# Optimization experiments

Hardware: AMD Instinct MI355X
Metric: run time of the kernel (lower is better)

The kernel has to match this reference:

```python
import jax, jax.numpy as jnp
import numpy as np

KNN_K = 3
EPS = 1e-8


def _make_poses(key, batch):
    """Random valid SE(3) matrices [B,4,4] (rotation via QR, small translation)."""
    k1, k2 = jax.random.split(key)
    A = jax.random.normal(k1, (batch, 3, 3), dtype=jnp.float32)
    Q, _ = jnp.linalg.qr(A)
    det = jnp.linalg.det(Q)[:, None, None]
    Q = Q * jnp.where(det < 0, -1.0, 1.0)  # ensure proper rotation
    t = jax.random.normal(k2, (batch, 3), dtype=jnp.float32) * 0.5
    pose = jnp.tile(jnp.eye(4, dtype=jnp.float32), (batch, 1, 1))
    pose = pose.at[:, :3, :3].set(Q)
    pose = pose.at[:, :3, 3].set(t)
    return pose


def setup_inputs() -> dict:
    key = jax.random.key(0)
    kq, kr, kf, kp0, kp1 = jax.random.split(key, 5)
    B, N, M = 2, 8192, 8192
    pc0 = jax.random.normal(kq, (B, N, 3), dtype=jnp.float32) * 20.0
    pc1 = jax.random.normal(kr, (B, M, 3), dtype=jnp.float32) * 20.0
    flow1 = jax.random.normal(kf, (B, M, 3), dtype=jnp.float32)
    pose0 = _make_poses(kp0, B)
    pose1 = _make_poses(kp1, B)
    return {"pc0": pc0, "pc1": pc1, "flow1": flow1, "pose0": pose0, "pose1": pose1}


def reference(pc0, pc1, flow1, pose0, pose1):
    # cal_pose0to1: transform from pc0 ego frame into pc1 ego frame
    pose_0to1 = jnp.linalg.inv(pose1) @ pose0            # [B,4,4]
    R = pose_0to1[:, :3, :3]                             # [B,3,3]
    t = pose_0to1[:, :3, 3]                              # [B,3]
    # pc0_in_pc1 = pc0 @ R^T + t
    pc0_t = jnp.einsum("bij,bnj->bni", R, pc0) + t[:, None, :]  # [B,N,3]
    pose_flow = pc0_t - pc0                              # ego-motion displacement

    # pairwise squared distances (cdist^2) via GEMM form: [B,N,M]
    q2 = jnp.sum(pc0_t * pc0_t, axis=-1)                 # [B,N]
    r2 = jnp.sum(pc1 * pc1, axis=-1)                     # [B,M]
    cross = jnp.einsum("bnd,bmd->bnm", pc0_t, pc1)
    d2 = q2[:, :, None] + r2[:, None, :] - 2.0 * cross

    # KNN: k smallest distances
    neg_d2, idx = jax.lax.top_k(-d2, KNN_K)              # [B,N,k]
    d = jnp.sqrt(jnp.maximum(-neg_d2, 0.0))

    # inverse-distance weights over the k neighbors
    w = 1.0 / (d + EPS)
    w = w / jnp.sum(w, axis=-1, keepdims=True)           # [B,N,k]

    # gather neighbor flows: flow1 [B,M,3] -> [B,N,k,3]
    gathered = jnp.take_along_axis(flow1[:, None, :, :], idx[..., None], axis=2)
    flow_interp = jnp.sum(w[..., None] * gathered, axis=2)  # [B,N,3]
    return flow_interp, pose_flow
```

## Files before the change

### kernel.cpp

```cpp
#include <hip/hip_runtime.h>
#include <math.h>
#include <float.h>
#include <limits.h>

#define CS   128
#define CT   16
#define TILE_PTS (CT * CS)
#define CSP  129
#define QB1  64
#define QT   16
#define MARGIN 0.05f
typedef unsigned long long ull;
#define KMAX 0xFFFFFFFFFFFFFFFFull

__device__ __forceinline__ unsigned int ford(float f) {
    unsigned int b = __float_as_uint(f);
    return b ^ (((unsigned int)((int)b >> 31)) | 0x80000000u);
}
__device__ __forceinline__ float funord(unsigned int u) {
    unsigned int m = ((u >> 31) - 1u) | 0x80000000u;
    return __uint_as_float(u ^ m);
}

__device__ __forceinline__ ull umin64(ull a, ull b) { return a < b ? a : b; }
__device__ __forceinline__ ull umax64(ull a, ull b) { return a > b ? a : b; }

__device__ __forceinline__ void ins3k(ull k, ull& k0, ull& k1, ull& k2) {
    ull n2 = umax64(k1, umin64(k2, k));
    ull n1 = umax64(k0, umin64(k1, k));
    k0 = umin64(k0, k);
    k1 = n1;
    k2 = n2;
}

__device__ __forceinline__ void sins(float d, float& a0, float& a1, float& a2)
{
    float n1 = __builtin_amdgcn_fmed3f(a0, a1, d);
    float n2 = __builtin_amdgcn_fmed3f(a1, a2, d);
    a0 = fminf(a0, d);
    a1 = n1;
    a2 = n2;
}

__device__ __forceinline__ void pose_rel(const float* __restrict__ P0,
                                         const float* __restrict__ P1,
                                         float R[3][3], float tv[3])
{
    float dt0 = P0[3]  - P1[3];
    float dt1 = P0[7]  - P1[7];
    float dt2 = P0[11] - P1[11];
    #pragma unroll
    for (int i = 0; i < 3; ++i) {
        float a0 = P1[i], a1 = P1[4 + i], a2 = P1[8 + i];
        #pragma unroll
        for (int j = 0; j < 3; ++j)
            R[i][j] = fmaf(a2, P0[8 + j], fmaf(a1, P0[4 + j], a0 * P0[j]));
        tv[i] = fmaf(a2, dt2, fmaf(a1, dt1, a0 * dt0));
    }
}

__launch_bounds__(256, 4)
__global__ void knn_phaseA(const float* __restrict__ pc0,
                           const float* __restrict__ pc1,
                           const float* __restrict__ pose0,
                           const float* __restrict__ pose1,
                           float* __restrict__ cmin,
                           int B, int N, int M, int cstride)
{
    __shared__ float4 tile[CT * CSP];
    __shared__ float4 qd[QB1];

    const int tid = threadIdx.x;
    const int b   = blockIdx.z;
    const int ctb = blockIdx.y;
    const int qb  = blockIdx.x * QB1;
    const int pbase = ctb * TILE_PTS;

    if (tid < QB1) {
        float R[3][3], tv[3];
        pose_rel(pose0 + b * 16, pose1 + b * 16, R, tv);
        int qg0 = qb + tid;
        int qg  = (qg0 < N) ? qg0 : (N - 1);
        const float px = pc0[(size_t)(b * N + qg) * 3 + 0];
        const float py = pc0[(size_t)(b * N + qg) * 3 + 1];
        const float pz = pc0[(size_t)(b * N + qg) * 3 + 2];
        float qx = fmaf(R[0][2], pz, fmaf(R[0][1], py, R[0][0] * px)) + tv[0];
        float qy = fmaf(R[1][2], pz, fmaf(R[1][1], py, R[1][0] * px)) + tv[1];
        float qz = fmaf(R[2][2], pz, fmaf(R[2][1], py, R[2][0] * px)) + tv[2];
        qd[tid] = make_float4(qx, qy, qz,
                              (qx * qx + qy * qy) + qz * qz);
    }

    #pragma unroll
    for (int k = 0; k < TILE_PTS / (256 * 4); ++k) {
        const int pl = (tid + k * 256) * 4;
        const int p  = pbase + pl;
        float4* dst = &tile[(pl >> 7) * CSP + (pl & (CS - 1))];
        if (p + 3 < M) {
            const float4* pf = (const float4*)(pc1 + (size_t)(b * M + p) * 3);
            float4 A = pf[0], Bv = pf[1], C = pf[2];
            dst[0] = make_float4(-2.f * A.x, -2.f * A.y, -2.f * A.z,
                                 (A.x * A.x + A.y * A.y) + A.z * A.z);
            dst[1] = make_float4(-2.f * A.w, -2.f * Bv.x, -2.f * Bv.y,
                                 (A.w * A.w + Bv.x * Bv.x) + Bv.y * Bv.y);
            dst[2] = make_float4(-2.f * Bv.z, -2.f * Bv.w, -2.f * C.x,
                                 (Bv.z * Bv.z + Bv.w * Bv.w) + C.x * C.x);
            dst[3] = make_float4(-2.f * C.y, -2.f * C.z, -2.f * C.w,
                                 (C.y * C.y + C.z * C.z) + C.w * C.w);
        } else {
            #pragma unroll
            for (int u = 0; u < 4; ++u) {
                int pp = p + u;
                float4 v;
                if (pp < M) {
                    const float* s = pc1 + (size_t)(b * M + pp) * 3;
                    float x = s[0], y = s[1], z = s[2];
                    v = make_float4(-2.f * x, -2.f * y, -2.f * z,
                                    (x * x + y * y) + z * z);
                } else {
                    v = make_float4(0.f, 0.f, 0.f, FLT_MAX);
                }
                dst[u] = v;
            }
        }
    }
    __syncthreads();

    const int w    = tid >> 6;
    const int lane = tid & 63;
    const int cl   = lane & 15;
    const int part = lane >> 4;

    float4 qv[QT];
    #pragma unroll
    for (int t = 0; t < QT; ++t) qv[t] = qd[w * QT + t];

    float mm[QT];
    #pragma unroll
    for (int t = 0; t < QT; ++t) mm[t] = FLT_MAX;

    const float4* tp = &tile[cl * CSP + part * 32];
    #pragma unroll 4
    for (int i = 0; i < 32; ++i) {
        const float4 v = tp[i];
        #pragma unroll
        for (int t = 0; t < QT; ++t)
            mm[t] = fminf(mm[t],
                fmaf(qv[t].x, v.x, fmaf(qv[t].y, v.y, fmaf(qv[t].z, v.z, v.w))));
    }

    #pragma unroll
    for (int msk = 16; msk <= 32; msk <<= 1) {
        #pragma unroll
        for (int t = 0; t < QT; ++t)
            mm[t] = fminf(mm[t], __shfl_xor(mm[t], msk));
    }

    if (part == 0) {
        const int cg = ctb * CT + cl;
        #pragma unroll
        for (int t = 0; t < QT; ++t) {
            int qg0 = qb + w * QT + t;
            int qg  = (qg0 < N) ? qg0 : (N - 1);
            cmin[((size_t)b * N + qg) * cstride + cg] = mm[t];
        }
    }
}

__launch_bounds__(256, 8)
__global__ void knn_select(const float* __restrict__ pc0,
                           const float* __restrict__ pc1,
                           const float* __restrict__ flow1,
                           const float* __restrict__ pose0,
                           const float* __restrict__ pose1,
                           const float* __restrict__ cmin,
                           float* __restrict__ out,
                           int B, int N, int M, int cstride)
{
    const int tid  = threadIdx.x;
    const int w    = tid >> 6;
    const int lane = tid & 63;
    const int g    = lane >> 4;
    const int l    = lane & 15;
    const int b    = blockIdx.y;
    const int q0   = blockIdx.x * 16 + w * 4 + g;
    const bool qvalid = (q0 < N);
    const int q    = qvalid ? q0 : (N - 1);

    const int ncc = cstride;
    const size_t row = (size_t)(b * N + q) * cstride;
    float c0, c1, c2, c3;
    if (l * 4 + 3 < ncc) {
        float4 cv = *(const float4*)&cmin[row + l * 4];
        c0 = cv.x; c1 = cv.y; c2 = cv.z; c3 = cv.w;
    } else {
        c0 = (l * 4 + 0 < ncc) ? cmin[row + l * 4 + 0] : FLT_MAX;
        c1 = (l * 4 + 1 < ncc) ? cmin[row + l * 4 + 1] : FLT_MAX;
        c2 = (l * 4 + 2 < ncc) ? cmin[row + l * 4 + 2] : FLT_MAX;
        c3 = (l * 4 + 3 < ncc) ? cmin[row + l * 4 + 3] : FLT_MAX;
    }

    float R[3][3], tv[3];
    pose_rel(pose0 + b * 16, pose1 + b * 16, R, tv);
    const float px = pc0[(size_t)(b * N + q) * 3 + 0];
    const float py = pc0[(size_t)(b * N + q) * 3 + 1];
    const float pz = pc0[(size_t)(b * N + q) * 3 + 2];
    const float qx = fmaf(R[0][2], pz, fmaf(R[0][1], py, R[0][0] * px)) + tv[0];
    const float qy = fmaf(R[1][2], pz, fmaf(R[1][1], py, R[1][0] * px)) + tv[1];
    const float qz = fmaf(R[2][2], pz, fmaf(R[2][1], py, R[2][0] * px)) + tv[2];
    const float q2 = (qx * qx + qy * qy) + qz * qz;

    float a0 = FLT_MAX, a1 = FLT_MAX, a2 = FLT_MAX;
    sins(c0, a0, a1, a2);
    sins(c1, a0, a1, a2);
    sins(c2, a0, a1, a2);
    sins(c3, a0, a1, a2);
    #pragma unroll
    for (int msk = 1; msk <= 8; msk <<= 1) {
        float o0 = __shfl_xor(a0, msk);
        float o1 = __shfl_xor(a1, msk);
        float o2 = __shfl_xor(a2, msk);
        sins(o0, a0, a1, a2);
        sins(o1, a0, a1, a2);
        sins(o2, a0, a1, a2);
    }
    const float thr = a2 + MARGIN;

    ull mask = ((ull)(c0 <= thr) << (4 * l + 0))
             | ((ull)(c1 <= thr) << (4 * l + 1))
             | ((ull)(c2 <= thr) << (4 * l + 2))
             | ((ull)(c3 <= thr) << (4 * l + 3));
    #pragma unroll
    for (int msk = 1; msk <= 8; msk <<= 1)
        mask |= __shfl_xor(mask, msk);

    ull kA0 = KMAX, kA1 = KMAX, kA2 = KMAX;
    ull kB0 = KMAX, kB1 = KMAX, kB2 = KMAX;
    while (mask) {
        const int ck = (int)__builtin_ctzll(mask);
        mask &= mask - 1;
        #pragma unroll
        for (int r = 0; r < CS / 16; ++r) {
            const int m = ck * CS + r * 16 + l;
            if (m < M) {
                const float* pp = pc1 + (size_t)(b * M + m) * 3;
                float x = pp[0], y = pp[1], z = pp[2];
                float r2 = (x * x + y * y) + z * z;
                float cr = fmaf(qz, z, fmaf(qy, y, qx * x));
                float dd = fmaf(-2.0f, cr, q2 + r2);
                ull kk = ((ull)ford(dd) << 32) | (unsigned int)m;
                if (r & 1) ins3k(kk, kB0, kB1, kB2);
                else       ins3k(kk, kA0, kA1, kA2);
            }
        }
    }
    ins3k(kB0, kA0, kA1, kA2);
    ins3k(kB1, kA0, kA1, kA2);
    ins3k(kB2, kA0, kA1, kA2);

    #pragma unroll
    for (int msk = 1; msk <= 8; msk <<= 1) {
        ull o0 = __shfl_xor(kA0, msk);
        ull o1 = __shfl_xor(kA1, msk);
        ull o2 = __shfl_xor(kA2, msk);
        ins3k(o0, kA0, kA1, kA2);
        ins3k(o1, kA0, kA1, kA2);
        ins3k(o2, kA0, kA1, kA2);
    }

    if (l == 0 && qvalid) {
        size_t pf = (size_t)B * N * 3 + (size_t)(b * N + q) * 3;
        out[pf + 0] = qx - px;
        out[pf + 1] = qy - py;
        out[pf + 2] = qz - pz;

        float D0 = funord((unsigned int)(kA0 >> 32));
        float D1 = funord((unsigned int)(kA1 >> 32));
        float D2 = funord((unsigned int)(kA2 >> 32));
        int   i0 = (int)(unsigned int)kA0;
        int   i1 = (int)(unsigned int)kA1;
        int   i2 = (int)(unsigned int)kA2;

        float dd0 = sqrtf(fmaxf(D0, 0.f));
        float dd1 = sqrtf(fmaxf(D1, 0.f));
        float dd2 = sqrtf(fmaxf(D2, 0.f));
        float w0 = 1.0f / (dd0 + 1e-8f);
        float w1 = 1.0f / (dd1 + 1e-8f);
        float w2 = 1.0f / (dd2 + 1e-8f);
        float wsum = (w0 + w1) + w2;
        w0 /= wsum; w1 /= wsum; w2 /= wsum;

        const float* f0 = flow1 + (size_t)(b * M + i0) * 3;
        const float* f1 = flow1 + (size_t)(b * M + i1) * 3;
        const float* f2 = flow1 + (size_t)(b * M + i2) * 3;

        const size_t ob = (size_t)(b * N + q) * 3;
        #pragma unroll
        for (int c = 0; c < 3; ++c) {
            float p0 = w0 * f0[c];
            float p1 = w1 * f1[c];
            float p2 = w2 * f2[c];
            out[ob + c] = (p0 + p1) + p2;
        }
    }
}

extern "C" void kernel_launch(void* const* d_in, const int* in_sizes, int n_in,
                              void* d_out, int out_size, void* d_ws, size_t ws_size,
                              hipStream_t stream) {
    const float* pc0   = (const float*)d_in[0];
    const float* pc1   = (const float*)d_in[1];
    const float* flow1 = (const float*)d_in[2];
    const float* pose0 = (const float*)d_in[3];
    const float* pose1 = (const float*)d_in[4];
    float* out = (float*)d_out;

    const int B = in_sizes[3] / 16;
    const int N = in_sizes[0] / (3 * B);
    const int M = in_sizes[1] / (3 * B);

    const int nct     = (M + TILE_PTS - 1) / TILE_PTS;
    const int cstride = nct * CT;

    float* cmin = (float*)d_ws;

    dim3 g1((N + QB1 - 1) / QB1, nct, B);
    knn_phaseA<<<g1, dim3(256), 0, stream>>>(pc0, pc1, pose0, pose1,
                                             cmin, B, N, M, cstride);

    dim3 g2((N + 15) / 16, B);
    knn_select<<<g2, dim3(256), 0, stream>>>(pc0, pc1, flow1, pose0, pose1,
                                             cmin, out, B, N, M, cstride);
}
```

Measured before the change: 34.07 us.

## Refine KNN pruning to 32-point sub-chunks with precomputed float4 point tile

Phase A now writes a per-query minimum for each 32-point sub-chunk instead of each 128-point chunk, and the first query block also stores the transformed pc1 points (-2x, -2y, -2z, r2) into a float4 workspace. The select kernel builds a small per-query list of candidate sub-chunks in shared memory with atomics and scans only those, reading the precomputed float4 points. If the list overflows it falls back to scanning every point. The aim is fewer candidate distance evaluations and cheaper loads in the select pass. In exchange, phase A writes four times as many minima and skips its shuffle reduction, and the select pass adds atomics and a brute-force fallback path.

```diff
diff --git a/kernel.cpp b/kernel.cpp
--- a/kernel.cpp
+++ b/kernel.cpp
@@ -4,11 +4,13 @@
 #include <limits.h>
 
 #define CS   128
+#define SUBS 32
 #define CT   16
 #define TILE_PTS (CT * CS)
 #define CSP  129
 #define QB1  64
 #define QT   16
+#define LCAP 12
 #define MARGIN 0.05f
 typedef unsigned long long ull;
 #define KMAX 0xFFFFFFFFFFFFFFFFull
@@ -64,8 +66,9 @@
                            const float* __restrict__ pc1,
                            const float* __restrict__ pose0,
                            const float* __restrict__ pose1,
-                           float* __restrict__ cmin,
-                           int B, int N, int M, int cstride)
+                           float* __restrict__ submin,
+                           float4* __restrict__ ptile,
+                           int B, int N, int M, int nsub)
 {
     __shared__ float4 tile[CT * CSP];
     __shared__ float4 qd[QB1];
@@ -91,36 +94,49 @@
                               (qx * qx + qy * qy) + qz * qz);
     }
 
+    const bool wr = (blockIdx.x == 0);
     #pragma unroll
     for (int k = 0; k < TILE_PTS / (256 * 4); ++k) {
         const int pl = (tid + k * 256) * 4;
         const int p  = pbase + pl;
         float4* dst = &tile[(pl >> 7) * CSP + (pl & (CS - 1))];
+        float4 w0, w1, w2, w3;
         if (p + 3 < M) {
             const float4* pf = (const float4*)(pc1 + (size_t)(b * M + p) * 3);
             float4 A = pf[0], Bv = pf[1], C = pf[2];
-            dst[0] = make_float4(-2.f * A.x, -2.f * A.y, -2.f * A.z,
-                                 (A.x * A.x + A.y * A.y) + A.z * A.z);
-            dst[1] = make_float4(-2.f * A.w, -2.f * Bv.x, -2.f * Bv.y,
-                                 (A.w * A.w + Bv.x * Bv.x) + Bv.y * Bv.y);
-            dst[2] = make_float4(-2.f * Bv.z, -2.f * Bv.w, -2.f * C.x,
-                                 (Bv.z * Bv.z + Bv.w * Bv.w) + C.x * C.x);
-            dst[3] = make_float4(-2.f * C.y, -2.f * C.z, -2.f * C.w,
-                                 (C.y * C.y + C.z * C.z) + C.w * C.w);
+            w0 = make_float4(-2.f * A.x, -2.f * A.y, -2.f * A.z,
+                             (A.x * A.x + A.y * A.y) + A.z * A.z);
+            w1 = make_float4(-2.f * A.w, -2.f * Bv.x, -2.f * Bv.y,
+                             (A.w * A.w + Bv.x * Bv.x) + Bv.y * Bv.y);
+            w2 = make_float4(-2.f * Bv.z, -2.f * Bv.w, -2.f * C.x,
+                             (Bv.z * Bv.z + Bv.w * Bv.w) + C.x * C.x);
+            w3 = make_float4(-2.f * C.y, -2.f * C.z, -2.f * C.w,
+                             (C.y * C.y + C.z * C.z) + C.w * C.w);
         } else {
+            float4 tmp[4];
             #pragma unroll
             for (int u = 0; u < 4; ++u) {
                 int pp = p + u;
-                float4 v;
                 if (pp < M) {
                     const float* s = pc1 + (size_t)(b * M + pp) * 3;
                     float x = s[0], y = s[1], z = s[2];
-                    v = make_float4(-2.f * x, -2.f * y, -2.f * z,
-                                    (x * x + y * y) + z * z);
+                    tmp[u] = make_float4(-2.f * x, -2.f * y, -2.f * z,
+                                         (x * x + y * y) + z * z);
                 } else {
-                    v = make_float4(0.f, 0.f, 0.f, FLT_MAX);
+                    tmp[u] = make_float4(0.f, 0.f, 0.f, FLT_MAX);
                 }
-                dst[u] = v;
+            }
+            w0 = tmp[0]; w1 = tmp[1]; w2 = tmp[2]; w3 = tmp[3];
+        }
+        dst[0] = w0; dst[1] = w1; dst[2] = w2; dst[3] = w3;
+        if (wr) {
+            float4* gp = &ptile[(size_t)b * M + p];
+            if (p + 3 < M) { gp[0] = w0; gp[1] = w1; gp[2] = w2; gp[3] = w3; }
+            else {
+                if (p + 0 < M) gp[0] = w0;
+                if (p + 1 < M) gp[1] = w1;
+                if (p + 2 < M) gp[2] = w2;
+                if (p + 3 < M) gp[3] = w3;
             }
         }
     }
@@ -149,55 +165,48 @@
                 fmaf(qv[t].x, v.x, fmaf(qv[t].y, v.y, fmaf(qv[t].z, v.z, v.w))));
     }
 
-    #pragma unroll
-    for (int msk = 16; msk <= 32; msk <<= 1) {
-        #pragma unroll
-        for (int t = 0; t < QT; ++t)
-            mm[t] = fminf(mm[t], __shfl_xor(mm[t], msk));
-    }
-
-    if (part == 0) {
-        const int cg = ctb * CT + cl;
-        #pragma unroll
-        for (int t = 0; t < QT; ++t) {
-            int qg0 = qb + w * QT + t;
-            int qg  = (qg0 < N) ? qg0 : (N - 1);
-            cmin[((size_t)b * N + qg) * cstride + cg] = mm[t];
-        }
+    const int sg = (ctb * CT + cl) * 4 + part;
+    #pragma unroll
+    for (int t = 0; t < QT; ++t) {
+        int qg0 = qb + w * QT + t;
+        int qg  = (qg0 < N) ? qg0 : (N - 1);
+        submin[((size_t)b * N + qg) * nsub + sg] = mm[t];
     }
 }
 
 __launch_bounds__(256, 8)
 __global__ void knn_select(const float* __restrict__ pc0,
-                           const float* __restrict__ pc1,
                            const float* __restrict__ flow1,
                            const float* __restrict__ pose0,
                            const float* __restrict__ pose1,
-                           const float* __restrict__ cmin,
+                           const float* __restrict__ submin,
+                           const float4* __restrict__ ptile,
                            float* __restrict__ out,
-                           int B, int N, int M, int cstride)
+                           int B, int N, int M, int nsub)
 {
+    __shared__ unsigned char list[16][LCAP];
+    __shared__ int cnt[16];
+
     const int tid  = threadIdx.x;
     const int w    = tid >> 6;
     const int lane = tid & 63;
     const int g    = lane >> 4;
     const int l    = lane & 15;
+    const int qi   = w * 4 + g;
     const int b    = blockIdx.y;
-    const int q0   = blockIdx.x * 16 + w * 4 + g;
+    const int q0   = blockIdx.x * 16 + qi;
     const bool qvalid = (q0 < N);
     const int q    = qvalid ? q0 : (N - 1);
 
-    const int ncc = cstride;
-    const size_t row = (size_t)(b * N + q) * cstride;
-    float c0, c1, c2, c3;
-    if (l * 4 + 3 < ncc) {
-        float4 cv = *(const float4*)&cmin[row + l * 4];
-        c0 = cv.x; c1 = cv.y; c2 = cv.z; c3 = cv.w;
-    } else {
-        c0 = (l * 4 + 0 < ncc) ? cmin[row + l * 4 + 0] : FLT_MAX;
-        c1 = (l * 4 + 1 < ncc) ? cmin[row + l * 4 + 1] : FLT_MAX;
-        c2 = (l * 4 + 2 < ncc) ? cmin[row + l * 4 + 2] : FLT_MAX;
-        c3 = (l * 4 + 3 < ncc) ? cmin[row + l * 4 + 3] : FLT_MAX;
+    const size_t row = (size_t)(b * N + q) * nsub;
+    const int sbase = l * 16;
+    float4 sA, sB, sC, sD;
+    {
+        const float4 FM = make_float4(FLT_MAX, FLT_MAX, FLT_MAX, FLT_MAX);
+        sA = (sbase +  3 < nsub) ? *(const float4*)&submin[row + sbase +  0] : FM;
+        sB = (sbase +  7 < nsub) ? *(const float4*)&submin[row + sbase +  4] : FM;
+        sC = (sbase + 11 < nsub) ? *(const float4*)&submin[row + sbase +  8] : FM;
+        sD = (sbase + 15 < nsub) ? *(const float4*)&submin[row + sbase + 12] : FM;
     }
 
     float R[3][3], tv[3];
@@ -210,6 +219,10 @@
     const float qz = fmaf(R[2][2], pz, fmaf(R[2][1], py, R[2][0] * px)) + tv[2];
     const float q2 = (qx * qx + qy * qy) + qz * qz;
 
+    float c0 = fminf(fminf(sA.x, sA.y), fminf(sA.z, sA.w));
+    float c1 = fminf(fminf(sB.x, sB.y), fminf(sB.z, sB.w));
+    float c2 = fminf(fminf(sC.x, sC.y), fminf(sC.z, sC.w));
+    float c3 = fminf(fminf(sD.x, sD.y), fminf(sD.z, sD.w));
     float a0 = FLT_MAX, a1 = FLT_MAX, a2 = FLT_MAX;
     sins(c0, a0, a1, a2);
     sins(c1, a0, a1, a2);
@@ -226,32 +239,56 @@
     }
     const float thr = a2 + MARGIN;
 
-    ull mask = ((ull)(c0 <= thr) << (4 * l + 0))
-             | ((ull)(c1 <= thr) << (4 * l + 1))
-             | ((ull)(c2 <= thr) << (4 * l + 2))
-             | ((ull)(c3 <= thr) << (4 * l + 3));
-    #pragma unroll
-    for (int msk = 1; msk <= 8; msk <<= 1)
-        mask |= __shfl_xor(mask, msk);
+    if (l == 0) cnt[qi] = 0;
+    {
+        float sv[16] = {sA.x, sA.y, sA.z, sA.w, sB.x, sB.y, sB.z, sB.w,
+                        sC.x, sC.y, sC.z, sC.w, sD.x, sD.y, sD.z, sD.w};
+        #pragma unroll
+        for (int j = 0; j < 16; ++j) {
+            if (sv[j] <= thr) {
+                int s = atomicAdd(&cnt[qi], 1);
+                if (s < LCAP) list[qi][s] = (unsigned char)(sbase + j);
+            }
+        }
+    }
+    const int c = cnt[qi];
+
+    unsigned int L0 = *(const unsigned int*)&list[qi][0];
+    unsigned int L1 = *(const unsigned int*)&list[qi][4];
+    unsigned int L2 = *(const unsigned int*)&list[qi][8];
 
     ull kA0 = KMAX, kA1 = KMAX, kA2 = KMAX;
     ull kB0 = KMAX, kB1 = KMAX, kB2 = KMAX;
-    while (mask) {
-        const int ck = (int)__builtin_ctzll(mask);
-        mask &= mask - 1;
-        #pragma unroll
-        for (int r = 0; r < CS / 16; ++r) {
-            const int m = ck * CS + r * 16 + l;
-            if (m < M) {
-                const float* pp = pc1 + (size_t)(b * M + m) * 3;
-                float x = pp[0], y = pp[1], z = pp[2];
-                float r2 = (x * x + y * y) + z * z;
-                float cr = fmaf(qz, z, fmaf(qy, y, qx * x));
-                float dd = fmaf(-2.0f, cr, q2 + r2);
-                ull kk = ((ull)ford(dd) << 32) | (unsigned int)m;
-                if (r & 1) ins3k(kk, kB0, kB1, kB2);
-                else       ins3k(kk, kA0, kA1, kA2);
+    const float4* pt = &ptile[(size_t)b * M];
+    if (c <= LCAP) {
+        #pragma unroll
+        for (int i = 0; i < LCAP; ++i) {
+            if (i < c) {
+                unsigned int word = (i < 4) ? L0 : (i < 8) ? L1 : L2;
+                int sub = (word >> (8 * (i & 3))) & 0xFF;
+                #pragma unroll
+                for (int r = 0; r < SUBS / 16; ++r) {
+                    const int m = sub * SUBS + r * 16 + l;
+                    if (m < M) {
+                        const float4 v = pt[m];
+                        float t  = fmaf(qz, v.z, fmaf(qy, v.y, qx * v.x));
+                        float dd = (q2 + v.w) + t;
+                        ull kk = ((ull)ford(dd) << 32) | (unsigned int)m;
+                        if (r & 1) ins3k(kk, kB0, kB1, kB2);
+                        else       ins3k(kk, kA0, kA1, kA2);
+                    }
+                }
             }
+        }
+    } else {
+        int par = 0;
+        for (int m = l; m < M; m += 16, par ^= 1) {
+            const float4 v = pt[m];
+            float t  = fmaf(qz, v.z, fmaf(qy, v.y, qx * v.x));
+            float dd = (q2 + v.w) + t;
+            ull kk = ((ull)ford(dd) << 32) | (unsigned int)m;
+            if (par) ins3k(kk, kB0, kB1, kB2);
+            else     ins3k(kk, kA0, kA1, kA2);
         }
     }
     ins3k(kB0, kA0, kA1, kA2);
@@ -296,11 +333,11 @@
 
         const size_t ob = (size_t)(b * N + q) * 3;
         #pragma unroll
-        for (int c = 0; c < 3; ++c) {
-            float p0 = w0 * f0[c];
-            float p1 = w1 * f1[c];
-            float p2 = w2 * f2[c];
-            out[ob + c] = (p0 + p1) + p2;
+        for (int ch = 0; ch < 3; ++ch) {
+            float p0 = w0 * f0[ch];
+            float p1 = w1 * f1[ch];
+            float p2 = w2 * f2[ch];
+            out[ob + ch] = (p0 + p1) + p2;
         }
     }
 }
@@ -319,16 +356,17 @@
     const int N = in_sizes[0] / (3 * B);
     const int M = in_sizes[1] / (3 * B);
 
-    const int nct     = (M + TILE_PTS - 1) / TILE_PTS;
-    const int cstride = nct * CT;
-
-    float* cmin = (float*)d_ws;
+    const int nct  = (M + TILE_PTS - 1) / TILE_PTS;
+    const int nsub = nct * CT * 4;
+
+    float*  submin = (float*)d_ws;
+    float4* ptile  = (float4*)((char*)d_ws + (size_t)B * N * nsub * sizeof(float));
 
     dim3 g1((N + QB1 - 1) / QB1, nct, B);
     knn_phaseA<<<g1, dim3(256), 0, stream>>>(pc0, pc1, pose0, pose1,
-                                             cmin, B, N, M, cstride);
+                                             submin, ptile, B, N, M, nsub);
 
     dim3 g2((N + 15) / 16, B);
-    knn_select<<<g2, dim3(256), 0, stream>>>(pc0, pc1, flow1, pose0, pose1,
-                                             cmin, out, B, N, M, cstride);
-}
+    knn_select<<<g2, dim3(256), 0, stream>>>(pc0, flow1, pose0, pose1,
+                                             submin, ptile, out, B, N, M, nsub);
+}
```

Result: slower. 39.84 us (+16.9%).

## Halve chunk size to 64 points with two 64-bit candidate masks

Applied to the files above, without the earlier changes.

Cuts the coarse chunk size from 128 to 64 points, so each query gets 128 chunk minima instead of 64. The selection kernel reads 8 minima per lane and builds two 64-bit masks. The finer pruning should mean fewer candidate points get rescanned in the exact top-3 pass. In exchange the cmin buffer doubles in size, the threshold step does more work, and the new code assumes cstride is exactly 128, with no bounds fallback for other M.

```diff
diff --git a/kernel.cpp b/kernel.cpp
--- a/kernel.cpp
+++ b/kernel.cpp
@@ -3,10 +3,10 @@
 #include <float.h>
 #include <limits.h>
 
-#define CS   128
-#define CT   16
+#define CS   64
+#define CT   32
 #define TILE_PTS (CT * CS)
-#define CSP  129
+#define CSP  65
 #define QB1  64
 #define QT   16
 #define MARGIN 0.05f
@@ -95,7 +95,7 @@
     for (int k = 0; k < TILE_PTS / (256 * 4); ++k) {
         const int pl = (tid + k * 256) * 4;
         const int p  = pbase + pl;
-        float4* dst = &tile[(pl >> 7) * CSP + (pl & (CS - 1))];
+        float4* dst = &tile[(pl >> 6) * CSP + (pl & (CS - 1))];
         if (p + 3 < M) {
             const float4* pf = (const float4*)(pc1 + (size_t)(b * M + p) * 3);
             float4 A = pf[0], Bv = pf[1], C = pf[2];
@@ -128,8 +128,8 @@
 
     const int w    = tid >> 6;
     const int lane = tid & 63;
-    const int cl   = lane & 15;
-    const int part = lane >> 4;
+    const int cl   = lane & 31;
+    const int part = lane >> 5;
 
     float4 qv[QT];
     #pragma unroll
@@ -150,11 +150,8 @@
     }
 
     #pragma unroll
-    for (int msk = 16; msk <= 32; msk <<= 1) {
-        #pragma unroll
-        for (int t = 0; t < QT; ++t)
-            mm[t] = fminf(mm[t], __shfl_xor(mm[t], msk));
-    }
+    for (int t = 0; t < QT; ++t)
+        mm[t] = fminf(mm[t], __shfl_xor(mm[t], 32));
 
     if (part == 0) {
         const int cg = ctb * CT + cl;
@@ -187,18 +184,9 @@
     const bool qvalid = (q0 < N);
     const int q    = qvalid ? q0 : (N - 1);
 
-    const int ncc = cstride;
     const size_t row = (size_t)(b * N + q) * cstride;
-    float c0, c1, c2, c3;
-    if (l * 4 + 3 < ncc) {
-        float4 cv = *(const float4*)&cmin[row + l * 4];
-        c0 = cv.x; c1 = cv.y; c2 = cv.z; c3 = cv.w;
-    } else {
-        c0 = (l * 4 + 0 < ncc) ? cmin[row + l * 4 + 0] : FLT_MAX;
-        c1 = (l * 4 + 1 < ncc) ? cmin[row + l * 4 + 1] : FLT_MAX;
-        c2 = (l * 4 + 2 < ncc) ? cmin[row + l * 4 + 2] : FLT_MAX;
-        c3 = (l * 4 + 3 < ncc) ? cmin[row + l * 4 + 3] : FLT_MAX;
-    }
+    const float4 sA = *(const float4*)&cmin[row + l * 8];
+    const float4 sB = *(const float4*)&cmin[row + l * 8 + 4];
 
     float R[3][3], tv[3];
     pose_rel(pose0 + b * 16, pose1 + b * 16, R, tv);
@@ -211,10 +199,10 @@
     const float q2 = (qx * qx + qy * qy) + qz * qz;
 
     float a0 = FLT_MAX, a1 = FLT_MAX, a2 = FLT_MAX;
-    sins(c0, a0, a1, a2);
-    sins(c1, a0, a1, a2);
-    sins(c2, a0, a1, a2);
-    sins(c3, a0, a1, a2);
+    sins(sA.x, a0, a1, a2); sins(sA.y, a0, a1, a2);
+    sins(sA.z, a0, a1, a2); sins(sA.w, a0, a1, a2);
+    sins(sB.x, a0, a1, a2); sins(sB.y, a0, a1, a2);
+    sins(sB.z, a0, a1, a2); sins(sB.w, a0, a1, a2);
     #pragma unroll
     for (int msk = 1; msk <= 8; msk <<= 1) {
         float o0 = __shfl_xor(a0, msk);
@@ -226,31 +214,42 @@
     }
     const float thr = a2 + MARGIN;
 
-    ull mask = ((ull)(c0 <= thr) << (4 * l + 0))
-             | ((ull)(c1 <= thr) << (4 * l + 1))
-             | ((ull)(c2 <= thr) << (4 * l + 2))
-             | ((ull)(c3 <= thr) << (4 * l + 3));
-    #pragma unroll
-    for (int msk = 1; msk <= 8; msk <<= 1)
-        mask |= __shfl_xor(mask, msk);
+    unsigned int mbits =
+          ((unsigned int)(sA.x <= thr) << 0) | ((unsigned int)(sA.y <= thr) << 1)
+        | ((unsigned int)(sA.z <= thr) << 2) | ((unsigned int)(sA.w <= thr) << 3)
+        | ((unsigned int)(sB.x <= thr) << 4) | ((unsigned int)(sB.y <= thr) << 5)
+        | ((unsigned int)(sB.z <= thr) << 6) | ((unsigned int)(sB.w <= thr) << 7);
+    ull m0 = (l < 8) ? ((ull)mbits << (8 * l)) : 0ull;
+    ull m1 = (l >= 8) ? ((ull)mbits << (8 * (l - 8))) : 0ull;
+    #pragma unroll
+    for (int msk = 1; msk <= 8; msk <<= 1) {
+        m0 |= __shfl_xor(m0, msk);
+        m1 |= __shfl_xor(m1, msk);
+    }
 
     ull kA0 = KMAX, kA1 = KMAX, kA2 = KMAX;
     ull kB0 = KMAX, kB1 = KMAX, kB2 = KMAX;
-    while (mask) {
-        const int ck = (int)__builtin_ctzll(mask);
-        mask &= mask - 1;
-        #pragma unroll
-        for (int r = 0; r < CS / 16; ++r) {
-            const int m = ck * CS + r * 16 + l;
-            if (m < M) {
-                const float* pp = pc1 + (size_t)(b * M + m) * 3;
-                float x = pp[0], y = pp[1], z = pp[2];
-                float r2 = (x * x + y * y) + z * z;
-                float cr = fmaf(qz, z, fmaf(qy, y, qx * x));
-                float dd = fmaf(-2.0f, cr, q2 + r2);
-                ull kk = ((ull)ford(dd) << 32) | (unsigned int)m;
-                if (r & 1) ins3k(kk, kB0, kB1, kB2);
-                else       ins3k(kk, kA0, kA1, kA2);
+    #pragma unroll
+    for (int half = 0; half < 2; ++half) {
+        ull mask = half ? m1 : m0;
+        const int cbase = half * 64;
+        while (mask) {
+            const int ck = (int)__builtin_ctzll(mask);
+            mask &= mask - 1;
+            const int mb = (cbase + ck) * CS;
+            #pragma unroll
+            for (int r = 0; r < CS / 16; ++r) {
+                const int m = mb + r * 16 + l;
+                if (m < M) {
+                    const float* pp = pc1 + (size_t)(b * M + m) * 3;
+                    float x = pp[0], y = pp[1], z = pp[2];
+                    float r2 = (x * x + y * y) + z * z;
+                    float cr = fmaf(qz, z, fmaf(qy, y, qx * x));
+                    float dd = fmaf(-2.0f, cr, q2 + r2);
+                    ull kk = ((ull)ford(dd) << 32) | (unsigned int)m;
+                    if (r & 1) ins3k(kk, kB0, kB1, kB2);
+                    else       ins3k(kk, kA0, kA1, kA2);
+                }
             }
         }
     }
```

Result: no change. 34.59 us (+1.5%).
